# Optimization experiments

Hardware: AMD Instinct MI355X
Metric: run time of the kernel (lower is better)

The kernel has to match this reference:

```python
import jax, jax.numpy as jnp
import numpy as np

N_CELLS = 19683   # 27**3 lattice
K = 26            # Moore-neighborhood max_neighbors
D = 128           # state_size
HG = 64           # gating hidden
CNF_STEPS = 3     # integration_steps
DT = 0.1


def setup_inputs() -> dict:
    key = jax.random.key(0)
    ks = jax.random.split(key, 12)
    s = lambda fan_in: 1.0 / np.sqrt(fan_in)
    return {
        "current_state": jax.random.normal(ks[0], (N_CELLS, D), jnp.float32),
        "neighbor_states": jax.random.normal(ks[1], (N_CELLS, K, D), jnp.float32),
        "conn_type": jax.random.randint(ks[2], (N_CELLS, K), 0, 3, jnp.int32),
        "W_local": jax.random.normal(ks[3], (2 * D, D), jnp.float32) * s(2 * D),
        "b_local": jnp.zeros((D,), jnp.float32),
        "W_msg": jax.random.normal(ks[4], (2 * D, D), jnp.float32) * s(2 * D),
        "b_msg": jnp.zeros((D,), jnp.float32),
        "W_upd": jax.random.normal(ks[5], (2 * D, D), jnp.float32) * s(2 * D),
        "b_upd": jnp.zeros((D,), jnp.float32),
        "W_cnf": jax.random.normal(ks[6], (2 * D, D), jnp.float32) * s(2 * D),
        "b_cnf": jnp.zeros((D,), jnp.float32),
        "W_g1": jax.random.normal(ks[7], (D, HG), jnp.float32) * s(D),
        "b_g1": jnp.zeros((HG,), jnp.float32),
        "W_g2": jax.random.normal(ks[8], (HG, 3), jnp.float32) * s(HG),
        "b_g2": jnp.zeros((3,), jnp.float32),
    }


def _masked_mean(nbr, mask):
    # nbr: [N,K,D], mask: [N,K] float -> [N,D]
    cnt = jnp.maximum(mask.sum(-1, keepdims=True), 1.0)
    return jnp.einsum("nkd,nk->nd", nbr, mask) / cnt


def reference(current_state, neighbor_states, conn_type,
              W_local, b_local, W_msg, b_msg, W_upd, b_upd,
              W_cnf, b_cnf, W_g1, b_g1, W_g2, b_g2):
    cur = current_state                       # [N,D]
    nbr = neighbor_states                     # [N,K,D]
    m_l = (conn_type == 0).astype(cur.dtype)  # local mask   [N,K]
    m_f = (conn_type == 1).astype(cur.dtype)  # functional
    m_d = (conn_type == 2).astype(cur.dtype)  # distant

    # --- local expert: SimpleLinear over [cell, mean(local neighbors)] ---
    agg_l = _masked_mean(nbr, m_l)
    local_out = jnp.tanh(jnp.concatenate([cur, agg_l], -1) @ W_local + b_local)

    # --- functional expert: GNN message passing ---
    cur_b = jnp.broadcast_to(cur[:, None, :], nbr.shape)          # [N,K,D]
    edge_in = jnp.concatenate([cur_b, nbr], -1)                   # [N,K,2D]
    msgs = jax.nn.relu(edge_in @ W_msg + b_msg)                   # [N,K,D]
    agg_msg = _masked_mean(msgs, m_f)                             # [N,D]
    func_out = jnp.tanh(jnp.concatenate([cur, agg_msg], -1) @ W_upd + b_upd)

    # --- distant expert: lightweight CNF (fixed-step Euler) ---
    agg_d = _masked_mean(nbr, m_d)

    def euler_step(s, _):
        ds = jnp.tanh(jnp.concatenate([s, agg_d], -1) @ W_cnf + b_cnf)
        return s + DT * ds, None

    distant_out, _ = jax.lax.scan(euler_step, cur, None, length=CNF_STEPS)

    # --- gating network: softmax over 3 experts ---
    gates = jax.nn.softmax(jax.nn.relu(cur @ W_g1 + b_g1) @ W_g2 + b_g2, -1)  # [N,3]

    out = (gates[:, 0:1] * local_out
           + gates[:, 1:2] * func_out
           + gates[:, 2:3] * distant_out)
    return out
```

## Files before the change

### kernel.cpp

```cpp
#include <hip/hip_runtime.h>
#include <hip/hip_bf16.h>
#include <math.h>

#define NC 19683
#define KN 26
#define DD 128
#define HGN 64
#define LDSB 136
#define DTC 0.1f

using bf8v = __attribute__((ext_vector_type(8))) short;
using f4v  = __attribute__((ext_vector_type(4))) float;

__device__ __forceinline__ unsigned short f2bf(float x) {
    union { float f; unsigned u; } v; v.f = x;
    unsigned r = v.u + 0x7fffu + ((v.u >> 16) & 1u);
    return (unsigned short)(r >> 16);
}
__device__ __forceinline__ unsigned pk2(float a, float b) {
    return ((unsigned)f2bf(a)) | (((unsigned)f2bf(b)) << 16);
}

__global__ __launch_bounds__(256) void k_prep(const float* __restrict__ Wl,
    const float* __restrict__ Wm, const float* __restrict__ Wu,
    const float* __restrict__ Wc, const float* __restrict__ Wg1,
    unsigned short* __restrict__ WT, unsigned short* __restrict__ WgT)
{
    int idx = blockIdx.x * 256 + threadIdx.x;
    if (idx < 131072) {
        int m = idx >> 15;
        int r = idx & 32767;
        int j = r >> 8;
        int i = r & 255;
        const float* src = (m == 0) ? Wl : (m == 1) ? Wm : (m == 2) ? Wu : Wc;
        WT[idx] = f2bf(src[i * DD + j]);
    } else {
        int idx2 = idx - 131072;
        int col = idx2 >> 7;
        int k = idx2 & 127;
        WgT[idx2] = f2bf(Wg1[k * HGN + col]);
    }
}

__global__ __launch_bounds__(256) void kA(const float* __restrict__ cur,
    const unsigned short* __restrict__ WT, const unsigned short* __restrict__ WgT,
    const float* __restrict__ b_msg, const float* __restrict__ bg1,
    const float* __restrict__ Wg2, const float* __restrict__ bg2,
    float* __restrict__ P, float* __restrict__ gates)
{
    __shared__ __align__(16) unsigned short Al[32][LDSB];
    __shared__ __align__(16) unsigned short Bl[128][LDSB];
    __shared__ __align__(16) unsigned short Gl[64][LDSB];
    __shared__ float hrelu[32][HGN + 4];
    int t = threadIdx.x;
    int n0 = blockIdx.x * 32;
    int w = t >> 6, lane = t & 63;
    int lm = lane & 15, lq = lane >> 4;

    for (int p = 0; p < 8; ++p) {
        int idx = p * 256 + t;
        int r = idx >> 6, c2 = (idx & 63) * 2;
        float2 v = {0.f, 0.f};
        if (n0 + r < NC) v = *(const float2*)&cur[(size_t)(n0 + r) * DD + c2];
        *(unsigned*)&Al[r][c2] = pk2(v.x, v.y);
    }
    const unsigned short* WmT = WT + 32768;
    for (int p = 0; p < 8; ++p) {
        int ch = p * 256 + t;
        int j = ch >> 4, i8 = (ch & 15) * 8;
        *(bf8v*)&Bl[j][i8] = *(const bf8v*)&WmT[j * 256 + i8];
    }
    for (int p = 0; p < 4; ++p) {
        int ch = p * 256 + t;
        int j = ch >> 4, i8 = (ch & 15) * 8;
        *(bf8v*)&Gl[j][i8] = *(const bf8v*)&WgT[j * 128 + i8];
    }
    __syncthreads();

    {
        int mt = w & 1, colh = w >> 1;
        for (int nt = 0; nt < 4; ++nt) {
            int col0 = colh * 64 + nt * 16;
            f4v acc = {0.f, 0.f, 0.f, 0.f};
            for (int s = 0; s < 4; ++s) {
                bf8v a = *(const bf8v*)&Al[mt * 16 + lm][s * 32 + lq * 8];
                bf8v b = *(const bf8v*)&Bl[col0 + lm][s * 32 + lq * 8];
                acc = __builtin_amdgcn_mfma_f32_16x16x32_bf16(a, b, acc, 0, 0, 0);
            }
            int col = col0 + lm;
            float bm = b_msg[col];
            for (int r = 0; r < 4; ++r) {
                int row = mt * 16 + lq * 4 + r;
                int n = n0 + row;
                if (n < NC) P[(size_t)n * DD + col] = acc[r] + bm;
            }
        }
    }
    {
        int col0 = w * 16;
        float bg = bg1[col0 + lm];
        for (int mt2 = 0; mt2 < 2; ++mt2) {
            f4v acc = {0.f, 0.f, 0.f, 0.f};
            for (int s = 0; s < 4; ++s) {
                bf8v a = *(const bf8v*)&Al[mt2 * 16 + lm][s * 32 + lq * 8];
                bf8v b = *(const bf8v*)&Gl[col0 + lm][s * 32 + lq * 8];
                acc = __builtin_amdgcn_mfma_f32_16x16x32_bf16(a, b, acc, 0, 0, 0);
            }
            for (int r = 0; r < 4; ++r)
                hrelu[mt2 * 16 + lq * 4 + r][col0 + lm] = fmaxf(acc[r] + bg, 0.f);
        }
    }
    __syncthreads();
    if (t < 32) {
        int n = n0 + t;
        if (n < NC) {
            float l[3];
            for (int e = 0; e < 3; ++e) {
                float s = bg2[e];
                for (int g = 0; g < HGN; ++g) s += hrelu[t][g] * Wg2[g * 3 + e];
                l[e] = s;
            }
            float m = fmaxf(l[0], fmaxf(l[1], l[2]));
            float e0 = expf(l[0] - m), e1 = expf(l[1] - m), e2 = expf(l[2] - m);
            float inv = 1.f / (e0 + e1 + e2);
            gates[n * 4 + 0] = e0 * inv;
            gates[n * 4 + 1] = e1 * inv;
            gates[n * 4 + 2] = e2 * inv;
        }
    }
}

__global__ __launch_bounds__(256) void kB(const float* __restrict__ nbr,
    const int* __restrict__ conn, const unsigned short* __restrict__ WT,
    const float* __restrict__ P, unsigned short* __restrict__ agg_l,
    unsigned short* __restrict__ agg_m, unsigned short* __restrict__ agg_d)
{
    __shared__ __align__(16) unsigned short Bl[128][LDSB];
    __shared__ __align__(16) unsigned short Al[4][32][LDSB];
    __shared__ float P8[4][DD];
    int t = threadIdx.x;
    int n0 = blockIdx.x * 4;
    int w = t >> 6, lane = t & 63;
    int n = n0 + w;
    bool act = n < NC;

    const unsigned short* Wm2T = WT + 32768 + 128;
    for (int p = 0; p < 8; ++p) {
        int ch = p * 256 + t;
        int j = ch >> 4, i8 = (ch & 15) * 8;
        *(bf8v*)&Bl[j][i8] = *(const bf8v*)&Wm2T[j * 256 + i8];
    }
    {
        int idx = t * 2;
        int r = idx >> 7, c = idx & 127;
        float2 v = {0.f, 0.f};
        if (n0 + r < NC) v = *(const float2*)&P[(size_t)(n0 + r) * DD + c];
        *(float2*)&P8[r][c] = v;
    }
    int ct = 3;
    if (act && lane < KN) ct = conn[(size_t)n * KN + lane];
    unsigned long long mlb = __ballot(ct == 0);
    unsigned long long mfb = __ballot(ct == 1);
    unsigned long long mdb = __ballot(ct == 2);
    float icl = 1.f / fmaxf((float)__builtin_popcountll(mlb), 1.f);
    float icf = 1.f / fmaxf((float)__builtin_popcountll(mfb), 1.f);
    float icd = 1.f / fmaxf((float)__builtin_popcountll(mdb), 1.f);

    int j2 = lane * 2;
    const float* base = nbr + ((size_t)(act ? n : 0) * KN) * DD + j2;
    float2 vv[KN];
    #pragma unroll
    for (int k = 0; k < KN; ++k) {
        float2 v = {0.f, 0.f};
        if (act) v = *(const float2*)&base[(size_t)k * DD];
        vv[k] = v;
    }
    float slx = 0.f, sly = 0.f, sdx = 0.f, sdy = 0.f;
    #pragma unroll
    for (int k = 0; k < KN; ++k) {
        float2 v = vv[k];
        if ((mlb >> k) & 1) { slx += v.x; sly += v.y; }
        if ((mdb >> k) & 1) { sdx += v.x; sdy += v.y; }
        *(unsigned*)&Al[w][k][j2] = pk2(v.x, v.y);
    }
    {
        unsigned* pz = (unsigned*)&Al[w][KN][0];
        for (int z = lane; z < (32 - KN) * LDSB / 2; z += 64) pz[z] = 0;
    }
    if (act) {
        *(unsigned*)&agg_l[(size_t)n * DD + j2] = pk2(slx * icl, sly * icl);
        *(unsigned*)&agg_d[(size_t)n * DD + j2] = pk2(sdx * icd, sdy * icd);
    }
    __syncthreads();

    if (act) {
        int lm = lane & 15, lq = lane >> 4;
        for (int nt = 0; nt < 8; ++nt) {
            int col0 = nt * 16;
            float pv = P8[w][col0 + lm];
            float msum = 0.f;
            for (int mt2 = 0; mt2 < 2; ++mt2) {
                f4v acc = {0.f, 0.f, 0.f, 0.f};
                for (int s = 0; s < 4; ++s) {
                    bf8v a = *(const bf8v*)&Al[w][mt2 * 16 + lm][s * 32 + lq * 8];
                    bf8v b = *(const bf8v*)&Bl[col0 + lm][s * 32 + lq * 8];
                    acc = __builtin_amdgcn_mfma_f32_16x16x32_bf16(a, b, acc, 0, 0, 0);
                }
                for (int r = 0; r < 4; ++r) {
                    int row = mt2 * 16 + lq * 4 + r;
                    if ((mfb >> row) & 1) msum += fmaxf(pv + acc[r], 0.f);
                }
            }
            msum += __shfl_xor(msum, 16, 64);
            msum += __shfl_xor(msum, 32, 64);
            if (lane < 16) agg_m[(size_t)n * DD + col0 + lane] = f2bf(msum * icf);
        }
    }
}

__global__ __launch_bounds__(256) void kC(const float* __restrict__ cur,
    const unsigned short* __restrict__ WT, const unsigned short* __restrict__ agg_l,
    const unsigned short* __restrict__ agg_m, const unsigned short* __restrict__ agg_d,
    const float* __restrict__ b_local, const float* __restrict__ b_upd,
    const float* __restrict__ b_cnf, const float* __restrict__ gates,
    float* __restrict__ out)
{
    __shared__ __align__(16) unsigned short Wl[128][LDSB];
    __shared__ __align__(16) unsigned short Xc[32][LDSB];
    __shared__ __align__(16) unsigned short Xa[32][LDSB];
    __shared__ float glds[32][4];
    __shared__ float bl[DD], bu[DD], bc[DD];
    int t = threadIdx.x;
    int n0 = blockIdx.x * 32;
    int w = t >> 6, lane = t & 63;
    int mt = w & 1, colh = w >> 1;
    int lm = lane & 15, lq = lane >> 4;

    auto stageW = [&](int m, int koff) {
        const unsigned short* src = WT + m * 32768 + koff;
        for (int p = 0; p < 8; ++p) {
            int ch = p * 256 + t;
            int j = ch >> 4, i8 = (ch & 15) * 8;
            *(bf8v*)&Wl[j][i8] = *(const bf8v*)&src[j * 256 + i8];
        }
    };
    auto stageXa = [&](const unsigned short* src) {
        for (int p = 0; p < 2; ++p) {
            int idx = p * 256 + t;
            int r = idx >> 4, c8 = (idx & 15) * 8;
            bf8v v = {0, 0, 0, 0, 0, 0, 0, 0};
            if (n0 + r < NC) v = *(const bf8v*)&src[(size_t)(n0 + r) * DD + c8];
            *(bf8v*)&Xa[r][c8] = v;
        }
    };
    auto mfmaPass = [&](unsigned short (&X)[32][LDSB], f4v* acc) {
        for (int nt = 0; nt < 4; ++nt) {
            int col0 = colh * 64 + nt * 16;
            for (int s = 0; s < 4; ++s) {
                bf8v a = *(const bf8v*)&X[mt * 16 + lm][s * 32 + lq * 8];
                bf8v b = *(const bf8v*)&Wl[col0 + lm][s * 32 + lq * 8];
                acc[nt] = __builtin_amdgcn_mfma_f32_16x16x32_bf16(a, b, acc[nt], 0, 0, 0);
            }
        }
    };

    for (int p = 0; p < 8; ++p) {
        int idx = p * 256 + t;
        int r = idx >> 6, c2 = (idx & 63) * 2;
        float2 v = {0.f, 0.f};
        if (n0 + r < NC) v = *(const float2*)&cur[(size_t)(n0 + r) * DD + c2];
        *(unsigned*)&Xc[r][c2] = pk2(v.x, v.y);
    }
    if (t < 128) { bl[t] = b_local[t]; bu[t] = b_upd[t]; bc[t] = b_cnf[t]; }
    if (t >= 128 && t < 160) {
        int r = t - 128; int n = n0 + r;
        float g0 = 0.f, g1 = 0.f, g2 = 0.f;
        if (n < NC) { g0 = gates[n * 4]; g1 = gates[n * 4 + 1]; g2 = gates[n * 4 + 2]; }
        glds[r][0] = g0; glds[r][1] = g1; glds[r][2] = g2;
    }
    stageW(0, 0);
    __syncthreads();

    f4v oacc[4], acc[4];
    for (int nt = 0; nt < 4; ++nt) oacc[nt] = (f4v){0.f, 0.f, 0.f, 0.f};

    for (int nt = 0; nt < 4; ++nt) acc[nt] = (f4v){0.f, 0.f, 0.f, 0.f};
    mfmaPass(Xc, acc);
    __syncthreads();
    stageW(0, 128); stageXa(agg_l);
    __syncthreads();
    mfmaPass(Xa, acc);
    for (int nt = 0; nt < 4; ++nt) {
        int col = colh * 64 + nt * 16 + lm;
        for (int r = 0; r < 4; ++r) {
            int row = mt * 16 + lq * 4 + r;
            oacc[nt][r] += glds[row][0] * tanhf(acc[nt][r] + bl[col]);
        }
    }

    __syncthreads();
    stageW(2, 0);
    __syncthreads();
    for (int nt = 0; nt < 4; ++nt) acc[nt] = (f4v){0.f, 0.f, 0.f, 0.f};
    mfmaPass(Xc, acc);
    __syncthreads();
    stageW(2, 128); stageXa(agg_m);
    __syncthreads();
    mfmaPass(Xa, acc);
    for (int nt = 0; nt < 4; ++nt) {
        int col = colh * 64 + nt * 16 + lm;
        for (int r = 0; r < 4; ++r) {
            int row = mt * 16 + lq * 4 + r;
            oacc[nt][r] += glds[row][1] * tanhf(acc[nt][r] + bu[col]);
        }
    }

    __syncthreads();
    stageW(3, 128); stageXa(agg_d);
    __syncthreads();
    for (int nt = 0; nt < 4; ++nt) acc[nt] = (f4v){0.f, 0.f, 0.f, 0.f};
    mfmaPass(Xa, acc);
    f4v hd[4], s[4];
    for (int nt = 0; nt < 4; ++nt) {
        int col = colh * 64 + nt * 16 + lm;
        for (int r = 0; r < 4; ++r) {
            int row = mt * 16 + lq * 4 + r;
            int n = n0 + row;
            hd[nt][r] = acc[nt][r] + bc[col];
            s[nt][r] = (n < NC) ? cur[(size_t)n * DD + col] : 0.f;
        }
    }
    __syncthreads();
    stageW(3, 0);
    for (int step = 0; step < 3; ++step) {
        for (int nt = 0; nt < 4; ++nt) {
            int col = colh * 64 + nt * 16 + lm;
            for (int r = 0; r < 4; ++r) {
                int row = mt * 16 + lq * 4 + r;
                Xa[row][col] = f2bf(s[nt][r]);
            }
        }
        __syncthreads();
        for (int nt = 0; nt < 4; ++nt) acc[nt] = (f4v){0.f, 0.f, 0.f, 0.f};
        mfmaPass(Xa, acc);
        for (int nt = 0; nt < 4; ++nt)
            for (int r = 0; r < 4; ++r)
                s[nt][r] += DTC * tanhf(acc[nt][r] + hd[nt][r]);
        __syncthreads();
    }

    for (int nt = 0; nt < 4; ++nt) {
        int col = colh * 64 + nt * 16 + lm;
        for (int r = 0; r < 4; ++r) {
            int row = mt * 16 + lq * 4 + r;
            int n = n0 + row;
            if (n < NC) out[(size_t)n * DD + col] = oacc[nt][r] + glds[row][2] * s[nt][r];
        }
    }
}

extern "C" void kernel_launch(void* const* d_in, const int* in_sizes, int n_in,
                              void* d_out, int out_size, void* d_ws, size_t ws_size,
                              hipStream_t stream) {
    const float* cur     = (const float*)d_in[0];
    const float* nbr     = (const float*)d_in[1];
    const int*   conn    = (const int*)d_in[2];
    const float* W_local = (const float*)d_in[3];
    const float* b_local = (const float*)d_in[4];
    const float* W_msg   = (const float*)d_in[5];
    const float* b_msg   = (const float*)d_in[6];
    const float* W_upd   = (const float*)d_in[7];
    const float* b_upd   = (const float*)d_in[8];
    const float* W_cnf   = (const float*)d_in[9];
    const float* b_cnf   = (const float*)d_in[10];
    const float* Wg1     = (const float*)d_in[11];
    const float* bg1     = (const float*)d_in[12];
    const float* Wg2     = (const float*)d_in[13];
    const float* bg2     = (const float*)d_in[14];
    float* out = (float*)d_out;

    char* ws = (char*)d_ws;
    unsigned short* WT  = (unsigned short*)ws;
    unsigned short* WgT = (unsigned short*)(ws + 262144);
    float* P      = (float*)(ws + 278528);
    float* gatesb = (float*)(ws + 278528 + 10077696);
    unsigned short* aggl = (unsigned short*)(ws + 278528 + 10077696 + 314928);
    unsigned short* aggm = aggl + (size_t)NC * DD;
    unsigned short* aggd = aggm + (size_t)NC * DD;

    hipLaunchKernelGGL(k_prep, dim3(544), dim3(256), 0, stream, W_local, W_msg, W_upd, W_cnf, Wg1, WT, WgT);
    hipLaunchKernelGGL(kA, dim3(616), dim3(256), 0, stream, cur, WT, WgT, b_msg, bg1, Wg2, bg2, P, gatesb);
    hipLaunchKernelGGL(kB, dim3(4921), dim3(256), 0, stream, nbr, conn, WT, P, aggl, aggm, aggd);
    hipLaunchKernelGGL(kC, dim3(616), dim3(256), 0, stream, cur, WT, aggl, aggm, aggd, b_local, b_upd, b_cnf, gatesb, out);
}
```

Before: 457.8 us.

## Make message kernel persistent with register-resident weights and use fast tanh

```diff
diff --git a/kernel.cpp b/kernel.cpp
--- a/kernel.cpp
+++ b/kernel.cpp
@@ -19,6 +19,11 @@
 }
 __device__ __forceinline__ unsigned pk2(float a, float b) {
     return ((unsigned)f2bf(a)) | (((unsigned)f2bf(b)) << 16);
+}
+__device__ __forceinline__ float ftanh(float x) {
+    float xc = fminf(fmaxf(x, -9.f), 9.f);
+    float z = __builtin_amdgcn_exp2f(xc * -2.885390081777927f);
+    return (1.f - z) * __builtin_amdgcn_rcpf(1.f + z);
 }
 
 __global__ __launch_bounds__(256) void k_prep(const float* __restrict__ Wl,
@@ -130,90 +135,84 @@
     }
 }
 
+#define KB_WAVES 2464
 __global__ __launch_bounds__(256) void kB(const float* __restrict__ nbr,
     const int* __restrict__ conn, const unsigned short* __restrict__ WT,
     const float* __restrict__ P, unsigned short* __restrict__ agg_l,
     unsigned short* __restrict__ agg_m, unsigned short* __restrict__ agg_d)
 {
-    __shared__ __align__(16) unsigned short Bl[128][LDSB];
     __shared__ __align__(16) unsigned short Al[4][32][LDSB];
     __shared__ float P8[4][DD];
     int t = threadIdx.x;
-    int n0 = blockIdx.x * 4;
     int w = t >> 6, lane = t & 63;
-    int n = n0 + w;
-    bool act = n < NC;
-
+    int lm = lane & 15, lq = lane >> 4;
+    int j2 = lane * 2;
+
+    bf8v bfr[8][4];
     const unsigned short* Wm2T = WT + 32768 + 128;
-    for (int p = 0; p < 8; ++p) {
-        int ch = p * 256 + t;
-        int j = ch >> 4, i8 = (ch & 15) * 8;
-        *(bf8v*)&Bl[j][i8] = *(const bf8v*)&Wm2T[j * 256 + i8];
-    }
-    {
-        int idx = t * 2;
-        int r = idx >> 7, c = idx & 127;
-        float2 v = {0.f, 0.f};
-        if (n0 + r < NC) v = *(const float2*)&P[(size_t)(n0 + r) * DD + c];
-        *(float2*)&P8[r][c] = v;
-    }
-    int ct = 3;
-    if (act && lane < KN) ct = conn[(size_t)n * KN + lane];
-    unsigned long long mlb = __ballot(ct == 0);
-    unsigned long long mfb = __ballot(ct == 1);
-    unsigned long long mdb = __ballot(ct == 2);
-    float icl = 1.f / fmaxf((float)__builtin_popcountll(mlb), 1.f);
-    float icf = 1.f / fmaxf((float)__builtin_popcountll(mfb), 1.f);
-    float icd = 1.f / fmaxf((float)__builtin_popcountll(mdb), 1.f);
-
-    int j2 = lane * 2;
-    const float* base = nbr + ((size_t)(act ? n : 0) * KN) * DD + j2;
-    float2 vv[KN];
     #pragma unroll
-    for (int k = 0; k < KN; ++k) {
-        float2 v = {0.f, 0.f};
-        if (act) v = *(const float2*)&base[(size_t)k * DD];
-        vv[k] = v;
-    }
-    float slx = 0.f, sly = 0.f, sdx = 0.f, sdy = 0.f;
-    #pragma unroll
-    for (int k = 0; k < KN; ++k) {
-        float2 v = vv[k];
-        if ((mlb >> k) & 1) { slx += v.x; sly += v.y; }
-        if ((mdb >> k) & 1) { sdx += v.x; sdy += v.y; }
-        *(unsigned*)&Al[w][k][j2] = pk2(v.x, v.y);
-    }
-    {
-        unsigned* pz = (unsigned*)&Al[w][KN][0];
-        for (int z = lane; z < (32 - KN) * LDSB / 2; z += 64) pz[z] = 0;
-    }
-    if (act) {
+    for (int nt = 0; nt < 8; ++nt)
+        #pragma unroll
+        for (int s = 0; s < 4; ++s)
+            bfr[nt][s] = *(const bf8v*)&Wm2T[(nt * 16 + lm) * 256 + s * 32 + lq * 8];
+
+    for (int n = blockIdx.x * 4 + w; n < NC; n += KB_WAVES) {
+        int ct = 3;
+        if (lane < KN) ct = conn[(size_t)n * KN + lane];
+        unsigned long long mlb = __ballot(ct == 0);
+        unsigned long long mfb = __ballot(ct == 1);
+        unsigned long long mdb = __ballot(ct == 2);
+        float icl = 1.f / fmaxf((float)__builtin_popcountll(mlb), 1.f);
+        float icf = 1.f / fmaxf((float)__builtin_popcountll(mfb), 1.f);
+        float icd = 1.f / fmaxf((float)__builtin_popcountll(mdb), 1.f);
+
+        *(float2*)&P8[w][j2] = *(const float2*)&P[(size_t)n * DD + j2];
+
+        const float* base = nbr + (size_t)n * KN * DD + j2;
+        float slx = 0.f, sly = 0.f, sdx = 0.f, sdy = 0.f;
+        #pragma unroll
+        for (int k = 0; k < KN; ++k) {
+            float2 v = *(const float2*)&base[(size_t)k * DD];
+            float fl = (float)((mlb >> k) & 1);
+            float fd = (float)((mdb >> k) & 1);
+            slx += fl * v.x; sly += fl * v.y;
+            sdx += fd * v.x; sdy += fd * v.y;
+            *(unsigned*)&Al[w][k][j2] = pk2(v.x, v.y);
+        }
+
         *(unsigned*)&agg_l[(size_t)n * DD + j2] = pk2(slx * icl, sly * icl);
         *(unsigned*)&agg_d[(size_t)n * DD + j2] = pk2(sdx * icd, sdy * icd);
-    }
-    __syncthreads();
-
-    if (act) {
-        int lm = lane & 15, lq = lane >> 4;
+
+        float msum[8];
+        #pragma unroll
+        for (int nt = 0; nt < 8; ++nt) msum[nt] = 0.f;
+        #pragma unroll
+        for (int mt = 0; mt < 2; ++mt) {
+            bf8v af[4];
+            #pragma unroll
+            for (int s = 0; s < 4; ++s)
+                af[s] = *(const bf8v*)&Al[w][mt * 16 + lm][s * 32 + lq * 8];
+            #pragma unroll
+            for (int nt = 0; nt < 8; ++nt) {
+                f4v acc = {0.f, 0.f, 0.f, 0.f};
+                #pragma unroll
+                for (int s = 0; s < 4; ++s)
+                    acc = __builtin_amdgcn_mfma_f32_16x16x32_bf16(af[s], bfr[nt][s], acc, 0, 0, 0);
+                float pv = P8[w][nt * 16 + lm];
+                #pragma unroll
+                for (int r = 0; r < 4; ++r) {
+                    int row = mt * 16 + lq * 4 + r;
+                    float fm = (float)((mfb >> row) & 1);
+                    msum[nt] += fm * fmaxf(pv + acc[r], 0.f);
+                }
+            }
+        }
+        #pragma unroll
         for (int nt = 0; nt < 8; ++nt) {
-            int col0 = nt * 16;
-            float pv = P8[w][col0 + lm];
-            float msum = 0.f;
-            for (int mt2 = 0; mt2 < 2; ++mt2) {
-                f4v acc = {0.f, 0.f, 0.f, 0.f};
-                for (int s = 0; s < 4; ++s) {
-                    bf8v a = *(const bf8v*)&Al[w][mt2 * 16 + lm][s * 32 + lq * 8];
-                    bf8v b = *(const bf8v*)&Bl[col0 + lm][s * 32 + lq * 8];
-                    acc = __builtin_amdgcn_mfma_f32_16x16x32_bf16(a, b, acc, 0, 0, 0);
-                }
-                for (int r = 0; r < 4; ++r) {
-                    int row = mt2 * 16 + lq * 4 + r;
-                    if ((mfb >> row) & 1) msum += fmaxf(pv + acc[r], 0.f);
-                }
-            }
-            msum += __shfl_xor(msum, 16, 64);
-            msum += __shfl_xor(msum, 32, 64);
-            if (lane < 16) agg_m[(size_t)n * DD + col0 + lane] = f2bf(msum * icf);
+            float m = msum[nt];
+            m += __shfl_xor(m, 16, 64);
+            m += __shfl_xor(m, 32, 64);
+            if (lane < 16) agg_m[(size_t)n * DD + nt * 16 + lane] = f2bf(m * icf);
         }
     }
 }
@@ -294,7 +293,7 @@
         int col = colh * 64 + nt * 16 + lm;
         for (int r = 0; r < 4; ++r) {
             int row = mt * 16 + lq * 4 + r;
-            oacc[nt][r] += glds[row][0] * tanhf(acc[nt][r] + bl[col]);
+            oacc[nt][r] += glds[row][0] * ftanh(acc[nt][r] + bl[col]);
         }
     }
 
@@ -311,7 +310,7 @@
         int col = colh * 64 + nt * 16 + lm;
         for (int r = 0; r < 4; ++r) {
             int row = mt * 16 + lq * 4 + r;
-            oacc[nt][r] += glds[row][1] * tanhf(acc[nt][r] + bu[col]);
+            oacc[nt][r] += glds[row][1] * ftanh(acc[nt][r] + bu[col]);
         }
     }
 
@@ -345,7 +344,7 @@
         mfmaPass(Xa, acc);
         for (int nt = 0; nt < 4; ++nt)
             for (int r = 0; r < 4; ++r)
-                s[nt][r] += DTC * tanhf(acc[nt][r] + hd[nt][r]);
+                s[nt][r] += DTC * ftanh(acc[nt][r] + hd[nt][r]);
         __syncthreads();
     }
 
@@ -390,6 +389,6 @@
 
     hipLaunchKernelGGL(k_prep, dim3(544), dim3(256), 0, stream, W_local, W_msg, W_upd, W_cnf, Wg1, WT, WgT);
     hipLaunchKernelGGL(kA, dim3(616), dim3(256), 0, stream, cur, WT, WgT, b_msg, bg1, Wg2, bg2, P, gatesb);
-    hipLaunchKernelGGL(kB, dim3(4921), dim3(256), 0, stream, nbr, conn, WT, P, aggl, aggm, aggd);
+    hipLaunchKernelGGL(kB, dim3(616), dim3(256), 0, stream, nbr, conn, WT, P, aggl, aggm, aggd);
     hipLaunchKernelGGL(kC, dim3(616), dim3(256), 0, stream, cur, WT, aggl, aggm, aggd, b_local, b_upd, b_cnf, gatesb, out);
 }
```

New measurement: 489.2 us. 1.07x slower.
